# Kernel tuning notes

Measured on AMD Instinct MI355X. Metric: run time of the kernel, lower is better.

## Reference

```python
import jax, jax.numpy as jnp
import numpy as np

D_MODEL = 1024
N_HEADS = 16
CAUSAL = True
NEG_INF = -1e10


def get_freqs(seq_len, n_dim):
    # standard RoPE frequencies: theta_i = 10000^(-2i/n_dim), angles[s, i] = s * theta_i
    inv_freq = 1.0 / (10000.0 ** (jnp.arange(0, n_dim, 2, dtype=jnp.float32) / n_dim))
    t = jnp.arange(seq_len, dtype=jnp.float32)
    return jnp.outer(t, inv_freq)  # [S, n_dim//2]


def rope(x, freqs):
    # x: [B, S, H, n_dim]; interleaved pair rotation
    B, S, H, Dh = x.shape
    xr = x.reshape(B, S, H, Dh // 2, 2)
    x1, x2 = xr[..., 0], xr[..., 1]
    cos = jnp.cos(freqs)[None, :, None, :]  # [1,S,1,Dh/2]
    sin = jnp.sin(freqs)[None, :, None, :]
    o1 = x1 * cos - x2 * sin
    o2 = x1 * sin + x2 * cos
    return jnp.stack([o1, o2], axis=-1).reshape(B, S, H, Dh)


def setup_inputs() -> dict:
    key = jax.random.key(0)
    ks = jax.random.split(key, 5)
    B, S, D = 2, 2048, D_MODEL
    return {
        "x": jax.random.normal(ks[0], (B, S, D), dtype=jnp.float32),
        "qw": jax.random.normal(ks[1], (D, D), dtype=jnp.float32),
        "kw": jax.random.normal(ks[2], (D, D), dtype=jnp.float32),
        "vw": jax.random.normal(ks[3], (D, D), dtype=jnp.float32),
        "ow": jax.random.normal(ks[4], (D, D), dtype=jnp.float32),
    }


def reference(x, qw, kw, vw, ow):
    B, S, D = x.shape
    H = N_HEADS
    Dh = D // H
    Q = (x @ qw).reshape(B, S, H, Dh)
    K = (x @ kw).reshape(B, S, H, Dh)
    V = (x @ vw).reshape(B, S, H, Dh)
    freqs = get_freqs(S, Dh)
    Q = rope(Q, freqs)
    K = rope(K, freqs)
    # [B,H,S,S] scores, scaled by sqrt(d_model) as in the original (not sqrt(head_dim))
    scores = jnp.einsum("bqhd,bkhd->bhqk", Q, K) / jnp.sqrt(jnp.float32(D))
    scores = scores.astype(jnp.float32)
    if CAUSAL:
        causal = jnp.tril(jnp.ones((S, S), dtype=bool))
        scores = jnp.where(causal[None, None, :, :], scores, NEG_INF)
    weights = jax.nn.softmax(scores, axis=-1)
    attn = jnp.einsum("bhqk,bkhd->bqhd", weights, V).reshape(B, S, D)
    return attn @ ow
```

## Files before the change

### kernel.cpp

```cpp
#include <hip/hip_runtime.h>
#include <hip/hip_bf16.h>
#include <math.h>

#define SEQ    2048
#define BATCH  2
#define DM     1024
#define NH     16
#define DH     64
#define BS_ROWS 4096
#define KDIM   1024

typedef __attribute__((ext_vector_type(8))) short short8v;
typedef __attribute__((ext_vector_type(4))) float f32x4;
typedef unsigned short ushort_t;

__device__ __forceinline__ unsigned short f2bf(float f) {
  union { float f; unsigned u; } v; v.f = f;
  unsigned r = (v.u + 0x7FFF + ((v.u >> 16) & 1)) >> 16;
  return (unsigned short)r;
}
__device__ __forceinline__ float bf2f(unsigned short h) {
  union { unsigned u; float f; } v; v.u = ((unsigned)h) << 16;
  return v.f;
}

__device__ __forceinline__ void gl16(const void* g, void* l) {
  __builtin_amdgcn_global_load_lds(
      (const __attribute__((address_space(1))) unsigned int*)g,
      (__attribute__((address_space(3))) unsigned int*)l,
      16, 0, 0);
}

__global__ __launch_bounds__(256)
void split_f32(const float* __restrict__ src, ushort_t* __restrict__ h,
               ushort_t* __restrict__ l, int n8)
{
  const int i = blockIdx.x * 256 + threadIdx.x;
  if (i >= n8) return;
  const float4 v0 = ((const float4*)src)[2 * i];
  const float4 v1 = ((const float4*)src)[2 * i + 1];
  const float vals[8] = {v0.x, v0.y, v0.z, v0.w, v1.x, v1.y, v1.z, v1.w};
  short8v hv, lv;
  #pragma unroll
  for (int e = 0; e < 8; e++) {
    const unsigned short hb = f2bf(vals[e]);
    hv[e] = (short)hb;
    lv[e] = (short)f2bf(vals[e] - bf2f(hb));
  }
  ((short8v*)h)[i] = hv;
  ((short8v*)l)[i] = lv;
}

__global__ __launch_bounds__(256)
void wtrans(const float* __restrict__ w0, const float* __restrict__ w1,
            const float* __restrict__ w2, const float* __restrict__ w3,
            ushort_t* __restrict__ WT)
{
  __shared__ float tile[64][65];
  const int z = blockIdx.z;
  const float* __restrict__ W = (z == 0) ? w0 : (z == 1) ? w1 : (z == 2) ? w2 : w3;
  ushort_t* __restrict__ Oh = WT + (size_t)z * 2097152;
  ushort_t* __restrict__ Ol = Oh + 1048576;

  const int n0 = blockIdx.x * 64, k0 = blockIdx.y * 64;
  const int r  = threadIdx.x >> 2;
  const int c0 = (threadIdx.x & 3) * 16;

  #pragma unroll
  for (int i = 0; i < 4; i++) {
    const float4 v = *(const float4*)&W[(size_t)(k0 + r) * KDIM + n0 + c0 + 4 * i];
    tile[r][c0 + 4 * i + 0] = v.x; tile[r][c0 + 4 * i + 1] = v.y;
    tile[r][c0 + 4 * i + 2] = v.z; tile[r][c0 + 4 * i + 3] = v.w;
  }
  __syncthreads();

  #pragma unroll
  for (int c = 0; c < 2; c++) {
    short8v hv, lv;
    #pragma unroll
    for (int e = 0; e < 8; e++) {
      const float x = tile[c0 + c * 8 + e][r];
      const unsigned short hb = f2bf(x);
      hv[e] = (short)hb;
      lv[e] = (short)f2bf(x - bf2f(hb));
    }
    const size_t off = (size_t)(n0 + r) * KDIM + k0 + c0 + c * 8;
    *(short8v*)&Oh[off] = hv;
    if (z <= 1) *(short8v*)&Ol[off] = lv;
  }
}

#define MF(a_, b_, c_) __builtin_amdgcn_mfma_f32_16x16x32_bf16(a_, b_, c_, 0, 0, 0)

#define M16(p_, q_)                                                          \
  c00=MF(p_##0,q_##0,c00); c01=MF(p_##0,q_##1,c01); c02=MF(p_##0,q_##2,c02); c03=MF(p_##0,q_##3,c03); \
  c10=MF(p_##1,q_##0,c10); c11=MF(p_##1,q_##1,c11); c12=MF(p_##1,q_##2,c12); c13=MF(p_##1,q_##3,c13); \
  c20=MF(p_##2,q_##0,c20); c21=MF(p_##2,q_##1,c21); c22=MF(p_##2,q_##2,c22); c23=MF(p_##2,q_##3,c23); \
  c30=MF(p_##3,q_##0,c30); c31=MF(p_##3,q_##1,c31); c32=MF(p_##3,q_##2,c32); c33=MF(p_##3,q_##3,c33);

__global__ __launch_bounds__(256, 2)
void gemm_qkv(const ushort_t* __restrict__ Ahp, const ushort_t* __restrict__ Alp,
              const ushort_t* __restrict__ WT,
              ushort_t* __restrict__ Qh, ushort_t* __restrict__ Ql,
              ushort_t* __restrict__ Kh, ushort_t* __restrict__ Kl,
              ushort_t* __restrict__ Vt)
{
  const int mode = blockIdx.z;
  const bool qk = (mode <= 1);
  const ushort_t* __restrict__ Bhp = WT + (size_t)mode * 2097152;
  const ushort_t* __restrict__ Blp = Bhp + 1048576;

  __shared__ ushort_t A2[128][64];
  __shared__ ushort_t B2[128][64];

  const int t = threadIdx.x;
  const int lane = t & 63, w = t >> 6;
  const int l4 = lane & 15, lh = lane >> 4;
  const int wm = w >> 1, wn = w & 1;

  const int lin = blockIdx.x + (blockIdx.y << 3);
  const int sw  = ((lin & 7) << 5) + (lin >> 3);
  const int row0 = (sw >> 3) * 128, col0 = (sw & 7) * 128;

  const int srow = t >> 3;
  const int spc  = t & 7;
  const int slc  = spc ^ (srow & 7);
  const int koff = (slc & 3) * 8;
  const ushort_t* __restrict__ sA = (slc < 4) ? Ahp : Alp;
  const ushort_t* __restrict__ sB = (slc < 4) ? Bhp : (qk ? Blp : Bhp);

  const int pcA = lh ^ (l4 & 7);

  f32x4 c00 = {0,0,0,0}, c01 = {0,0,0,0}, c02 = {0,0,0,0}, c03 = {0,0,0,0};
  f32x4 c10 = {0,0,0,0}, c11 = {0,0,0,0}, c12 = {0,0,0,0}, c13 = {0,0,0,0};
  f32x4 c20 = {0,0,0,0}, c21 = {0,0,0,0}, c22 = {0,0,0,0}, c23 = {0,0,0,0};
  f32x4 c30 = {0,0,0,0}, c31 = {0,0,0,0}, c32 = {0,0,0,0}, c33 = {0,0,0,0};

  const int rA = wm * 64 + l4;
  const int rB = wn * 64 + l4;

  const bool stageMe = qk || (slc < 4);

  for (int k0 = 0; k0 < KDIM; k0 += 32) {
    if (stageMe) {
      #pragma unroll
      for (int i = 0; i < 4; i++) {
        gl16(sA + (size_t)(row0 + i * 32 + srow) * KDIM + k0 + koff,
             (char*)A2 + i * 4096 + w * 1024);
        gl16(sB + (size_t)(col0 + i * 32 + srow) * KDIM + k0 + koff,
             (char*)B2 + i * 4096 + w * 1024);
      }
    }
    __syncthreads();

    const short8v ah0 = *(const short8v*)&A2[rA +  0][pcA * 8];
    const short8v ah1 = *(const short8v*)&A2[rA + 16][pcA * 8];
    const short8v ah2 = *(const short8v*)&A2[rA + 32][pcA * 8];
    const short8v ah3 = *(const short8v*)&A2[rA + 48][pcA * 8];
    const short8v bh0 = *(const short8v*)&B2[rB +  0][pcA * 8];
    const short8v bh1 = *(const short8v*)&B2[rB + 16][pcA * 8];
    const short8v bh2 = *(const short8v*)&B2[rB + 32][pcA * 8];
    const short8v bh3 = *(const short8v*)&B2[rB + 48][pcA * 8];

    M16(ah, bh)
    if (qk) {
      const short8v al0 = *(const short8v*)&A2[rA +  0][(pcA ^ 4) * 8];
      const short8v al1 = *(const short8v*)&A2[rA + 16][(pcA ^ 4) * 8];
      const short8v al2 = *(const short8v*)&A2[rA + 32][(pcA ^ 4) * 8];
      const short8v al3 = *(const short8v*)&A2[rA + 48][(pcA ^ 4) * 8];
      const short8v bl0 = *(const short8v*)&B2[rB +  0][(pcA ^ 4) * 8];
      const short8v bl1 = *(const short8v*)&B2[rB + 16][(pcA ^ 4) * 8];
      const short8v bl2 = *(const short8v*)&B2[rB + 32][(pcA ^ 4) * 8];
      const short8v bl3 = *(const short8v*)&B2[rB + 48][(pcA ^ 4) * 8];
      M16(ah, bl)
      M16(al, bh)
    }
    __syncthreads();
  }

  f32x4 acc[4][4];
  acc[0][0]=c00; acc[0][1]=c01; acc[0][2]=c02; acc[0][3]=c03;
  acc[1][0]=c10; acc[1][1]=c11; acc[1][2]=c12; acc[1][3]=c13;
  acc[2][0]=c20; acc[2][1]=c21; acc[2][2]=c22; acc[2][3]=c23;
  acc[3][0]=c30; acc[3][1]=c31; acc[3][2]=c32; acc[3][3]=c33;

  if (mode <= 1) {
    const float scale = (mode == 0) ? 0.03125f : 1.0f;
    ushort_t* __restrict__ Hp = (mode == 0) ? Qh : Kh;
    ushort_t* __restrict__ Lp = (mode == 0) ? Ql : Kl;
    #pragma unroll
    for (int mf = 0; mf < 4; mf++)
      #pragma unroll
      for (int nf = 0; nf < 4; nf++) {
        const int col = col0 + wn * 64 + nf * 16 + l4;
        const int p = (col & (DH - 1)) >> 1;
        const float fr = exp2f((float)p * -0.41524101186092030f);
        const float sgn = (col & 1) ? 1.0f : -1.0f;
        #pragma unroll
        for (int j = 0; j < 4; j++) {
          const int grow = row0 + wm * 64 + mf * 16 + lh * 4 + j;
          const float s = (float)(grow & (SEQ - 1));
          float sn, cs;
          sincosf(s * fr, &sn, &cs);
          const float val = acc[mf][nf][j];
          const float par = __shfl_xor(val, 1);
          const float out = val * cs + par * (sgn * sn);
          const float xsc = out * scale;
          const unsigned short hb = f2bf(xsc);
          Hp[(size_t)grow * DM + col] = hb;
          Lp[(size_t)grow * DM + col] = f2bf(xsc - bf2f(hb));
        }
      }
  } else {
    #pragma unroll
    for (int mf = 0; mf < 4; mf++)
      #pragma unroll
      for (int nf = 0; nf < 4; nf++) {
        const int col = col0 + wn * 64 + nf * 16 + l4;
        const int hh = col >> 6, dd = col & (DH - 1);
        #pragma unroll
        for (int j = 0; j < 4; j++) {
          const int grow = row0 + wm * 64 + mf * 16 + lh * 4 + j;
          const int b = grow >> 11, ss = grow & (SEQ - 1);
          Vt[((size_t)((b * NH + hh) * DH + dd)) * SEQ + ss] = f2bf(acc[mf][nf][j]);
        }
      }
  }
}

__global__ __launch_bounds__(256, 2)
void gemm_out(const ushort_t* __restrict__ Ahp, const ushort_t* __restrict__ WT,
              float* __restrict__ Cf)
{
  const ushort_t* __restrict__ Bhp = WT + (size_t)3 * 2097152;

  __shared__ ushort_t A3[128][32];
  __shared__ ushort_t B3[64][32];

  const int t = threadIdx.x;
  const int lane = t & 63, w = t >> 6;
  const int l4 = lane & 15, lh = lane >> 4;
  const int wm = w >> 1, wn = w & 1;

  const int lin = blockIdx.x + (blockIdx.y << 4);
  const int sw  = ((lin & 7) << 6) + (lin >> 3);
  const int row0 = (sw >> 4) * 128, col0 = (sw & 15) * 64;

  const int srow = t >> 2;
  const int spc  = t & 3;
  const int slc  = spc ^ (srow & 3);
  const int koff = slc * 8;

  const int pc4 = lh ^ (l4 & 3);

  f32x4 c00={0,0,0,0}, c01={0,0,0,0};
  f32x4 c10={0,0,0,0}, c11={0,0,0,0};
  f32x4 c20={0,0,0,0}, c21={0,0,0,0};
  f32x4 c30={0,0,0,0}, c31={0,0,0,0};

  const int rA = wm * 64 + l4;
  const int rB = wn * 32 + l4;

  for (int k0 = 0; k0 < KDIM; k0 += 32) {
    #pragma unroll
    for (int i = 0; i < 2; i++)
      gl16(Ahp + (size_t)(row0 + i * 64 + srow) * KDIM + k0 + koff,
           (char*)A3 + i * 4096 + w * 1024);
    gl16(Bhp + (size_t)(col0 + srow) * KDIM + k0 + koff,
         (char*)B3 + w * 1024);
    __syncthreads();

    const short8v ah0 = *(const short8v*)&A3[rA +  0][pc4 * 8];
    const short8v ah1 = *(const short8v*)&A3[rA + 16][pc4 * 8];
    const short8v ah2 = *(const short8v*)&A3[rA + 32][pc4 * 8];
    const short8v ah3 = *(const short8v*)&A3[rA + 48][pc4 * 8];
    const short8v bh0 = *(const short8v*)&B3[rB +  0][pc4 * 8];
    const short8v bh1 = *(const short8v*)&B3[rB + 16][pc4 * 8];

    c00 = MF(ah0, bh0, c00); c01 = MF(ah0, bh1, c01);
    c10 = MF(ah1, bh0, c10); c11 = MF(ah1, bh1, c11);
    c20 = MF(ah2, bh0, c20); c21 = MF(ah2, bh1, c21);
    c30 = MF(ah3, bh0, c30); c31 = MF(ah3, bh1, c31);
    __syncthreads();
  }

  f32x4 acc[4][2];
  acc[0][0]=c00; acc[0][1]=c01; acc[1][0]=c10; acc[1][1]=c11;
  acc[2][0]=c20; acc[2][1]=c21; acc[3][0]=c30; acc[3][1]=c31;

  #pragma unroll
  for (int mf = 0; mf < 4; mf++)
    #pragma unroll
    for (int nf = 0; nf < 2; nf++) {
      const int col = col0 + wn * 32 + nf * 16 + l4;
      #pragma unroll
      for (int j = 0; j < 4; j++) {
        const int grow = row0 + wm * 64 + mf * 16 + lh * 4 + j;
        Cf[(size_t)grow * DM + col] = acc[mf][nf][j];
      }
    }
}

__global__ __launch_bounds__(256, 4)
void attn_mfma(const ushort_t* __restrict__ Qh, const ushort_t* __restrict__ Ql,
               const ushort_t* __restrict__ Kh, const ushort_t* __restrict__ Kl,
               const ushort_t* __restrict__ Vt, ushort_t* __restrict__ AAh)
{
  __shared__ __align__(16) ushort_t Khl[2][2][64][32];
  __shared__ __align__(16) ushort_t Vtl[64][72];
  __shared__ __align__(16) ushort_t Pl[4][16][72];

  const int t = threadIdx.x;
  const int lane = t & 63, wv = t >> 6;
  const int l4 = lane & 15, lh = lane >> 4;

  const int lin = blockIdx.x + (blockIdx.y << 5);
  const int sw  = ((lin & 7) << 7) + (lin >> 3);
  const int qblk = sw & 31, bh = sw >> 5;

  const int bI = bh >> 4, h = bh & 15;
  const int q0w = qblk * 64 + wv * 16;
  const int qrow = q0w + l4;

  const int kr = t >> 2, kc = t & 3;
  const int ckw = (kc ^ ((kr >> 1) & 3)) * 8;
  const int csr = (lh ^ ((l4 >> 1) & 3)) * 8;

  short8v aqh0, aqh1, aql0, aql1;
  {
    const size_t qoff = (size_t)((bI * SEQ) + qrow) * DM + h * DH;
    aqh0 = *(const short8v*)&Qh[qoff + lh * 8];
    aqh1 = *(const short8v*)&Qh[qoff + 32 + lh * 8];
    aql0 = *(const short8v*)&Ql[qoff + lh * 8];
    aql1 = *(const short8v*)&Ql[qoff + 32 + lh * 8];
  }

  f32x4 o0 = {0,0,0,0}, o1 = {0,0,0,0}, o2 = {0,0,0,0}, o3 = {0,0,0,0};
  float mrun = -1e30f, lsum = 0.f;

  const ushort_t* __restrict__ Vg = Vt + (size_t)bh * DH * SEQ;
  const size_t kgbase = (size_t)(bI * SEQ + kr) * DM + h * DH + kc * 8;
  const int nt = qblk + 1;

  short8v rkh0, rkh1, rkl0, rkl1, rv0, rv1;

#define LOADR(kt_) {                                                         \
    const size_t ko = kgbase + (size_t)(kt_) * 64 * DM;                      \
    rkh0 = *(const short8v*)&Kh[ko];                                         \
    rkh1 = *(const short8v*)&Kh[ko + 32];                                    \
    rkl0 = *(const short8v*)&Kl[ko];                                         \
    rkl1 = *(const short8v*)&Kl[ko + 32];                                    \
    const size_t vo = (size_t)kr * SEQ + (kt_) * 64 + kc * 8;                \
    rv0 = *(const short8v*)&Vg[vo];                                          \
    rv1 = *(const short8v*)&Vg[vo + 32]; }

#define WRITES() {                                                           \
    *(short8v*)&Khl[0][0][kr][ckw] = rkh0;                                   \
    *(short8v*)&Khl[0][1][kr][ckw] = rkh1;                                   \
    *(short8v*)&Khl[1][0][kr][ckw] = rkl0;                                   \
    *(short8v*)&Khl[1][1][kr][ckw] = rkl1;                                   \
    *(short8v*)&Vtl[kr][kc * 8]      = rv0;                                  \
    *(short8v*)&Vtl[kr][kc * 8 + 32] = rv1; }

#define QKSTEP(sN, n) {                                                      \
    const short8v kh0 = *(const short8v*)&Khl[0][0][(n)*16 + l4][csr];       \
    const short8v kh1 = *(const short8v*)&Khl[0][1][(n)*16 + l4][csr];       \
    const short8v kl0 = *(const short8v*)&Khl[1][0][(n)*16 + l4][csr];       \
    const short8v kl1 = *(const short8v*)&Khl[1][1][(n)*16 + l4][csr];       \
    sN = MF(kh0, aqh0, sN);                                                  \
    sN = MF(kh0, aql0, sN);                                                  \
    sN = MF(kl0, aqh0, sN);                                                  \
    sN = MF(kh1, aqh1, sN);                                                  \
    sN = MF(kh1, aql1, sN);                                                  \
    sN = MF(kl1, aqh1, sN); }

#define MASKN(sN, n) {                                                       \
    const int kb0 = kb + (n)*16 + lh*4;                                      \
    if (kb0 + 0 > qrow) sN[0] = -1e30f;                                      \
    if (kb0 + 1 > qrow) sN[1] = -1e30f;                                      \
    if (kb0 + 2 > qrow) sN[2] = -1e30f;                                      \
    if (kb0 + 3 > qrow) sN[3] = -1e30f; }

#define EXPN(sN) {                                                           \
    sN[0] = __expf(sN[0] - nm); sN[1] = __expf(sN[1] - nm);                  \
    sN[2] = __expf(sN[2] - nm); sN[3] = __expf(sN[3] - nm); }

#define PWRITE(sN, n) {                                                      \
    unsigned pa, pb;                                                         \
    asm("v_cvt_pk_bf16_f32 %0, %1, %2" : "=v"(pa) : "v"(sN[0]), "v"(sN[1]));\
    asm("v_cvt_pk_bf16_f32 %0, %1, %2" : "=v"(pb) : "v"(sN[2]), "v"(sN[3]));\
    *(unsigned*)&Pl[wv][l4][(n)*16 + lh*4]     = pa;                         \
    *(unsigned*)&Pl[wv][l4][(n)*16 + lh*4 + 2] = pb; }

#define PVSTEP(kb2) {                                                        \
    const short8v ap  = *(const short8v*)&Pl[wv][l4][(kb2)*32 + lh*8];       \
    const short8v bv0 = *(const short8v*)&Vtl[ 0 + l4][(kb2)*32 + lh*8];     \
    const short8v bv1 = *(const short8v*)&Vtl[16 + l4][(kb2)*32 + lh*8];     \
    const short8v bv2 = *(const short8v*)&Vtl[32 + l4][(kb2)*32 + lh*8];     \
    const short8v bv3 = *(const short8v*)&Vtl[48 + l4][(kb2)*32 + lh*8];     \
    o0 = MF(bv0, ap, o0);                                                    \
    o1 = MF(bv1, ap, o1);                                                    \
    o2 = MF(bv2, ap, o2);                                                    \
    o3 = MF(bv3, ap, o3); }

  LOADR(0); WRITES();
  __syncthreads();

  for (int kt = 0; kt < nt; kt++) {
    const bool pf = (kt + 1 < nt);
    if (pf) LOADR(kt + 1);

    f32x4 s0 = {0,0,0,0}, s1 = {0,0,0,0}, s2 = {0,0,0,0}, s3 = {0,0,0,0};
    QKSTEP(s0, 0) QKSTEP(s1, 1) QKSTEP(s2, 2) QKSTEP(s3, 3)

    const int kb = kt * 64;
    MASKN(s0, 0) MASKN(s1, 1) MASKN(s2, 2) MASKN(s3, 3)

    float vmax = fmaxf(fmaxf(fmaxf(s0[0], s0[1]), fmaxf(s0[2], s0[3])),
                       fmaxf(fmaxf(s1[0], s1[1]), fmaxf(s1[2], s1[3])));
    vmax = fmaxf(vmax, fmaxf(fmaxf(s2[0], s2[1]), fmaxf(s2[2], s2[3])));
    vmax = fmaxf(vmax, fmaxf(fmaxf(s3[0], s3[1]), fmaxf(s3[2], s3[3])));
    vmax = fmaxf(vmax, __shfl_xor(vmax, 16));
    vmax = fmaxf(vmax, __shfl_xor(vmax, 32));

    float nm = fmaxf(mrun, vmax);
    if (__all(nm - mrun <= 8.0f)) {
      nm = mrun;
    } else {
      const float corr = __expf(mrun - nm);
      lsum *= corr;
      o0 *= corr; o1 *= corr; o2 *= corr; o3 *= corr;
      mrun = nm;
    }

    EXPN(s0) EXPN(s1) EXPN(s2) EXPN(s3)

    float rs = (s0[0] + s0[1]) + (s0[2] + s0[3]) + (s1[0] + s1[1]) + (s1[2] + s1[3])
             + (s2[0] + s2[1]) + (s2[2] + s2[3]) + (s3[0] + s3[1]) + (s3[2] + s3[3]);
    rs += __shfl_xor(rs, 16);
    rs += __shfl_xor(rs, 32);
    lsum += rs;

    PWRITE(s0, 0) PWRITE(s1, 1) PWRITE(s2, 2) PWRITE(s3, 3)

    PVSTEP(0) PVSTEP(1)

    if (pf) {
      __syncthreads();
      WRITES();
      __syncthreads();
    }
  }

  const float inv = 1.0f / lsum;
  const size_t rowoff = ((size_t)(bI * SEQ + qrow)) * DM + h * DH;
  #pragma unroll
  for (int df = 0; df < 4; df++) {
    const f32x4 ov = (df == 0) ? o0 : (df == 1) ? o1 : (df == 2) ? o2 : o3;
    #pragma unroll
    for (int jp = 0; jp < 2; jp++) {
      const float x0 = ov[2 * jp] * inv;
      const float x1 = ov[2 * jp + 1] * inv;
      const unsigned short h0 = f2bf(x0), h1 = f2bf(x1);
      const size_t col = rowoff + df * 16 + lh * 4 + 2 * jp;
      *(unsigned*)&AAh[col] = (unsigned)h0 | ((unsigned)h1 << 16);
    }
  }
#undef LOADR
#undef WRITES
#undef QKSTEP
#undef MASKN
#undef EXPN
#undef PWRITE
#undef PVSTEP
}

extern "C" void kernel_launch(void* const* d_in, const int* in_sizes, int n_in,
                              void* d_out, int out_size, void* d_ws, size_t ws_size,
                              hipStream_t stream) {
  const float* x  = (const float*)d_in[0];
  const float* qw = (const float*)d_in[1];
  const float* kw = (const float*)d_in[2];
  const float* vw = (const float*)d_in[3];
  const float* ow = (const float*)d_in[4];

  char* ws = (char*)d_ws;
  ushort_t* Xh  = (ushort_t*)ws;
  ushort_t* Xl  = Xh + 4194304;
  ushort_t* AAh = Xh;
  ushort_t* Kh  = (ushort_t*)(ws + (16u << 20));
  ushort_t* Kl  = Kh + 4194304;
  ushort_t* Vt  = (ushort_t*)(ws + (32u << 20));
  ushort_t* WT  = (ushort_t*)(ws + (40u << 20));
  ushort_t* Qh  = (ushort_t*)d_out;
  ushort_t* Ql  = Qh + 4194304;
  float*    out = (float*)d_out;

  split_f32<<<dim3(2048), dim3(256), 0, stream>>>(x, Xh, Xl, 524288);
  wtrans<<<dim3(16, 16, 4), dim3(256), 0, stream>>>(qw, kw, vw, ow, WT);
  gemm_qkv<<<dim3(8, 32, 3), dim3(256), 0, stream>>>(
      Xh, Xl, WT, Qh, Ql, Kh, Kl, Vt);
  attn_mfma<<<dim3(SEQ / 64, BATCH * NH), dim3(256), 0, stream>>>(
      Qh, Ql, Kh, Kl, Vt, AAh);
  gemm_out<<<dim3(16, 32), dim3(256), 0, stream>>>(AAh, WT, out);
}
```

Baseline: 199.0 us.

## Shrink QKV GEMM tile to 64x128 and add MFMA priority hints in attention

The QKV projection GEMM moves from 128x128 tiles with a 2x2 warp layout to 64x128 tiles with four warps split along N. Each warp now holds 8 accumulators instead of 16, launch bounds rise to 4 blocks per CU, and the grid doubles. The aim is higher occupancy and better load balance, at the cost of less reuse of the staged B tile and more global loads overall. Separately, the attention kernel wraps its QK and PV MFMA sections in s_setprio to favour matrix issue over other waves.

```diff
diff --git a/kernel.cpp b/kernel.cpp
--- a/kernel.cpp
+++ b/kernel.cpp
@@ -92,13 +92,7 @@
 
 #define MF(a_, b_, c_) __builtin_amdgcn_mfma_f32_16x16x32_bf16(a_, b_, c_, 0, 0, 0)
 
-#define M16(p_, q_)                                                          \
-  c00=MF(p_##0,q_##0,c00); c01=MF(p_##0,q_##1,c01); c02=MF(p_##0,q_##2,c02); c03=MF(p_##0,q_##3,c03); \
-  c10=MF(p_##1,q_##0,c10); c11=MF(p_##1,q_##1,c11); c12=MF(p_##1,q_##2,c12); c13=MF(p_##1,q_##3,c13); \
-  c20=MF(p_##2,q_##0,c20); c21=MF(p_##2,q_##1,c21); c22=MF(p_##2,q_##2,c22); c23=MF(p_##2,q_##3,c23); \
-  c30=MF(p_##3,q_##0,c30); c31=MF(p_##3,q_##1,c31); c32=MF(p_##3,q_##2,c32); c33=MF(p_##3,q_##3,c33);
-
-__global__ __launch_bounds__(256, 2)
+__global__ __launch_bounds__(256, 4)
 void gemm_qkv(const ushort_t* __restrict__ Ahp, const ushort_t* __restrict__ Alp,
               const ushort_t* __restrict__ WT,
               ushort_t* __restrict__ Qh, ushort_t* __restrict__ Ql,
@@ -110,95 +104,101 @@
   const ushort_t* __restrict__ Bhp = WT + (size_t)mode * 2097152;
   const ushort_t* __restrict__ Blp = Bhp + 1048576;
 
-  __shared__ ushort_t A2[128][64];
+  __shared__ ushort_t A2[64][64];
   __shared__ ushort_t B2[128][64];
 
   const int t = threadIdx.x;
   const int lane = t & 63, w = t >> 6;
   const int l4 = lane & 15, lh = lane >> 4;
-  const int wm = w >> 1, wn = w & 1;
+  const int wn = w;
 
   const int lin = blockIdx.x + (blockIdx.y << 3);
-  const int sw  = ((lin & 7) << 5) + (lin >> 3);
-  const int row0 = (sw >> 3) * 128, col0 = (sw & 7) * 128;
+  const int sw  = ((lin & 7) << 6) + (lin >> 3);
+  const int row0 = (sw >> 3) * 64, col0 = (sw & 7) * 128;
 
   const int srow = t >> 3;
   const int spc  = t & 7;
   const int slc  = spc ^ (srow & 7);
   const int koff = (slc & 3) * 8;
   const ushort_t* __restrict__ sA = (slc < 4) ? Ahp : Alp;
-  const ushort_t* __restrict__ sB = (slc < 4) ? Bhp : (qk ? Blp : Bhp);
+  const ushort_t* __restrict__ sB = (slc < 4) ? Bhp : Blp;
+  const bool stageMe = qk || (slc < 4);
 
   const int pcA = lh ^ (l4 & 7);
 
-  f32x4 c00 = {0,0,0,0}, c01 = {0,0,0,0}, c02 = {0,0,0,0}, c03 = {0,0,0,0};
-  f32x4 c10 = {0,0,0,0}, c11 = {0,0,0,0}, c12 = {0,0,0,0}, c13 = {0,0,0,0};
-  f32x4 c20 = {0,0,0,0}, c21 = {0,0,0,0}, c22 = {0,0,0,0}, c23 = {0,0,0,0};
-  f32x4 c30 = {0,0,0,0}, c31 = {0,0,0,0}, c32 = {0,0,0,0}, c33 = {0,0,0,0};
-
-  const int rA = wm * 64 + l4;
-  const int rB = wn * 64 + l4;
-
-  const bool stageMe = qk || (slc < 4);
+  f32x4 c00 = {0,0,0,0}, c01 = {0,0,0,0};
+  f32x4 c10 = {0,0,0,0}, c11 = {0,0,0,0};
+  f32x4 c20 = {0,0,0,0}, c21 = {0,0,0,0};
+  f32x4 c30 = {0,0,0,0}, c31 = {0,0,0,0};
+
+  const int rB0 = wn * 32 + l4;
+  const int rB1 = wn * 32 + 16 + l4;
 
   for (int k0 = 0; k0 < KDIM; k0 += 32) {
     if (stageMe) {
       #pragma unroll
-      for (int i = 0; i < 4; i++) {
+      for (int i = 0; i < 2; i++)
         gl16(sA + (size_t)(row0 + i * 32 + srow) * KDIM + k0 + koff,
              (char*)A2 + i * 4096 + w * 1024);
+      #pragma unroll
+      for (int i = 0; i < 4; i++)
         gl16(sB + (size_t)(col0 + i * 32 + srow) * KDIM + k0 + koff,
              (char*)B2 + i * 4096 + w * 1024);
-      }
     }
     __syncthreads();
 
-    const short8v ah0 = *(const short8v*)&A2[rA +  0][pcA * 8];
-    const short8v ah1 = *(const short8v*)&A2[rA + 16][pcA * 8];
-    const short8v ah2 = *(const short8v*)&A2[rA + 32][pcA * 8];
-    const short8v ah3 = *(const short8v*)&A2[rA + 48][pcA * 8];
-    const short8v bh0 = *(const short8v*)&B2[rB +  0][pcA * 8];
-    const short8v bh1 = *(const short8v*)&B2[rB + 16][pcA * 8];
-    const short8v bh2 = *(const short8v*)&B2[rB + 32][pcA * 8];
-    const short8v bh3 = *(const short8v*)&B2[rB + 48][pcA * 8];
-
-    M16(ah, bh)
+    const short8v ah0 = *(const short8v*)&A2[ 0 + l4][pcA * 8];
+    const short8v ah1 = *(const short8v*)&A2[16 + l4][pcA * 8];
+    const short8v ah2 = *(const short8v*)&A2[32 + l4][pcA * 8];
+    const short8v ah3 = *(const short8v*)&A2[48 + l4][pcA * 8];
+    const short8v bh0 = *(const short8v*)&B2[rB0][pcA * 8];
+    const short8v bh1 = *(const short8v*)&B2[rB1][pcA * 8];
+
+    c00 = MF(ah0, bh0, c00); c01 = MF(ah0, bh1, c01);
+    c10 = MF(ah1, bh0, c10); c11 = MF(ah1, bh1, c11);
+    c20 = MF(ah2, bh0, c20); c21 = MF(ah2, bh1, c21);
+    c30 = MF(ah3, bh0, c30); c31 = MF(ah3, bh1, c31);
+
     if (qk) {
-      const short8v al0 = *(const short8v*)&A2[rA +  0][(pcA ^ 4) * 8];
-      const short8v al1 = *(const short8v*)&A2[rA + 16][(pcA ^ 4) * 8];
-      const short8v al2 = *(const short8v*)&A2[rA + 32][(pcA ^ 4) * 8];
-      const short8v al3 = *(const short8v*)&A2[rA + 48][(pcA ^ 4) * 8];
-      const short8v bl0 = *(const short8v*)&B2[rB +  0][(pcA ^ 4) * 8];
-      const short8v bl1 = *(const short8v*)&B2[rB + 16][(pcA ^ 4) * 8];
-      const short8v bl2 = *(const short8v*)&B2[rB + 32][(pcA ^ 4) * 8];
-      const short8v bl3 = *(const short8v*)&B2[rB + 48][(pcA ^ 4) * 8];
-      M16(ah, bl)
-      M16(al, bh)
+      const short8v al0 = *(const short8v*)&A2[ 0 + l4][(pcA ^ 4) * 8];
+      const short8v al1 = *(const short8v*)&A2[16 + l4][(pcA ^ 4) * 8];
+      const short8v al2 = *(const short8v*)&A2[32 + l4][(pcA ^ 4) * 8];
+      const short8v al3 = *(const short8v*)&A2[48 + l4][(pcA ^ 4) * 8];
+      const short8v bl0 = *(const short8v*)&B2[rB0][(pcA ^ 4) * 8];
+      const short8v bl1 = *(const short8v*)&B2[rB1][(pcA ^ 4) * 8];
+
+      c00 = MF(ah0, bl0, c00); c01 = MF(ah0, bl1, c01);
+      c10 = MF(ah1, bl0, c10); c11 = MF(ah1, bl1, c11);
+      c20 = MF(ah2, bl0, c20); c21 = MF(ah2, bl1, c21);
+      c30 = MF(ah3, bl0, c30); c31 = MF(ah3, bl1, c31);
+
+      c00 = MF(al0, bh0, c00); c01 = MF(al0, bh1, c01);
+      c10 = MF(al1, bh0, c10); c11 = MF(al1, bh1, c11);
+      c20 = MF(al2, bh0, c20); c21 = MF(al2, bh1, c21);
+      c30 = MF(al3, bh0, c30); c31 = MF(al3, bh1, c31);
     }
     __syncthreads();
   }
 
-  f32x4 acc[4][4];
-  acc[0][0]=c00; acc[0][1]=c01; acc[0][2]=c02; acc[0][3]=c03;
-  acc[1][0]=c10; acc[1][1]=c11; acc[1][2]=c12; acc[1][3]=c13;
-  acc[2][0]=c20; acc[2][1]=c21; acc[2][2]=c22; acc[2][3]=c23;
-  acc[3][0]=c30; acc[3][1]=c31; acc[3][2]=c32; acc[3][3]=c33;
+  f32x4 acc[4][2];
+  acc[0][0]=c00; acc[0][1]=c01; acc[1][0]=c10; acc[1][1]=c11;
+  acc[2][0]=c20; acc[2][1]=c21; acc[3][0]=c30; acc[3][1]=c31;
 
   if (mode <= 1) {
     const float scale = (mode == 0) ? 0.03125f : 1.0f;
     ushort_t* __restrict__ Hp = (mode == 0) ? Qh : Kh;
     ushort_t* __restrict__ Lp = (mode == 0) ? Ql : Kl;
     #pragma unroll
-    for (int mf = 0; mf < 4; mf++)
+    for (int nf = 0; nf < 2; nf++) {
+      const int col = col0 + wn * 32 + nf * 16 + l4;
+      const int p = (col & (DH - 1)) >> 1;
+      const float fr = exp2f((float)p * -0.41524101186092030f);
+      const float sgn = (col & 1) ? 1.0f : -1.0f;
       #pragma unroll
-      for (int nf = 0; nf < 4; nf++) {
-        const int col = col0 + wn * 64 + nf * 16 + l4;
-        const int p = (col & (DH - 1)) >> 1;
-        const float fr = exp2f((float)p * -0.41524101186092030f);
-        const float sgn = (col & 1) ? 1.0f : -1.0f;
+      for (int mf = 0; mf < 4; mf++) {
         #pragma unroll
         for (int j = 0; j < 4; j++) {
-          const int grow = row0 + wm * 64 + mf * 16 + lh * 4 + j;
+          const int grow = row0 + mf * 16 + lh * 4 + j;
           const float s = (float)(grow & (SEQ - 1));
           float sn, cs;
           sincosf(s * fr, &sn, &cs);
@@ -211,20 +211,22 @@
           Lp[(size_t)grow * DM + col] = f2bf(xsc - bf2f(hb));
         }
       }
+    }
   } else {
     #pragma unroll
-    for (int mf = 0; mf < 4; mf++)
+    for (int nf = 0; nf < 2; nf++) {
+      const int col = col0 + wn * 32 + nf * 16 + l4;
+      const int hh = col >> 6, dd = col & (DH - 1);
       #pragma unroll
-      for (int nf = 0; nf < 4; nf++) {
-        const int col = col0 + wn * 64 + nf * 16 + l4;
-        const int hh = col >> 6, dd = col & (DH - 1);
+      for (int mf = 0; mf < 4; mf++) {
         #pragma unroll
         for (int j = 0; j < 4; j++) {
-          const int grow = row0 + wm * 64 + mf * 16 + lh * 4 + j;
+          const int grow = row0 + mf * 16 + lh * 4 + j;
           const int b = grow >> 11, ss = grow & (SEQ - 1);
           Vt[((size_t)((b * NH + hh) * DH + dd)) * SEQ + ss] = f2bf(acc[mf][nf][j]);
         }
       }
+    }
   }
 }
 
@@ -411,7 +413,9 @@
     if (pf) LOADR(kt + 1);
 
     f32x4 s0 = {0,0,0,0}, s1 = {0,0,0,0}, s2 = {0,0,0,0}, s3 = {0,0,0,0};
+    __builtin_amdgcn_s_setprio(1);
     QKSTEP(s0, 0) QKSTEP(s1, 1) QKSTEP(s2, 2) QKSTEP(s3, 3)
+    __builtin_amdgcn_s_setprio(0);
 
     const int kb = kt * 64;
     MASKN(s0, 0) MASKN(s1, 1) MASKN(s2, 2) MASKN(s3, 3)
@@ -443,7 +447,9 @@
 
     PWRITE(s0, 0) PWRITE(s1, 1) PWRITE(s2, 2) PWRITE(s3, 3)
 
+    __builtin_amdgcn_s_setprio(1);
     PVSTEP(0) PVSTEP(1)
+    __builtin_amdgcn_s_setprio(0);
 
     if (pf) {
       __syncthreads();
@@ -498,7 +504,7 @@
 
   split_f32<<<dim3(2048), dim3(256), 0, stream>>>(x, Xh, Xl, 524288);
   wtrans<<<dim3(16, 16, 4), dim3(256), 0, stream>>>(qw, kw, vw, ow, WT);
-  gemm_qkv<<<dim3(8, 32, 3), dim3(256), 0, stream>>>(
+  gemm_qkv<<<dim3(8, 64, 3), dim3(256), 0, stream>>>(
       Xh, Xl, WT, Qh, Ql, Kh, Kl, Vt);
   attn_mfma<<<dim3(SEQ / 64, BATCH * NH), dim3(256), 0, stream>>>(
       Qh, Ql, Kh, Kl, Vt, AAh);
```

After: 199.7 us. About the same (+0.4%).

## Merge prologue kernels, fold log2e into Q scale, add MFMA priority hints

Applied to the files above, without the earlier changes.

Combines the input split and weight transpose kernels into a single launch so one kernel launch and its gap go away. Folds log2(e) into the Q scale so softmax can use exp2f directly and skip the multiply inside __expf, with the rescale threshold adjusted to match. Wraps the QK and PV MFMA sections in s_setprio to favour matrix-issuing waves. Folding the constant into the bf16-split Q values may shift rounding slightly.

```diff
diff --git a/kernel.cpp b/kernel.cpp
--- a/kernel.cpp
+++ b/kernel.cpp
@@ -32,37 +32,41 @@
 }
 
 __global__ __launch_bounds__(256)
-void split_f32(const float* __restrict__ src, ushort_t* __restrict__ h,
-               ushort_t* __restrict__ l, int n8)
-{
-  const int i = blockIdx.x * 256 + threadIdx.x;
-  if (i >= n8) return;
-  const float4 v0 = ((const float4*)src)[2 * i];
-  const float4 v1 = ((const float4*)src)[2 * i + 1];
-  const float vals[8] = {v0.x, v0.y, v0.z, v0.w, v1.x, v1.y, v1.z, v1.w};
-  short8v hv, lv;
-  #pragma unroll
-  for (int e = 0; e < 8; e++) {
-    const unsigned short hb = f2bf(vals[e]);
-    hv[e] = (short)hb;
-    lv[e] = (short)f2bf(vals[e] - bf2f(hb));
-  }
-  ((short8v*)h)[i] = hv;
-  ((short8v*)l)[i] = lv;
-}
-
-__global__ __launch_bounds__(256)
-void wtrans(const float* __restrict__ w0, const float* __restrict__ w1,
-            const float* __restrict__ w2, const float* __restrict__ w3,
-            ushort_t* __restrict__ WT)
+void prologue(const float* __restrict__ x,
+              const float* __restrict__ w0, const float* __restrict__ w1,
+              const float* __restrict__ w2, const float* __restrict__ w3,
+              ushort_t* __restrict__ Xh, ushort_t* __restrict__ Xl,
+              ushort_t* __restrict__ WT)
 {
   __shared__ float tile[64][65];
-  const int z = blockIdx.z;
+  const int bid = blockIdx.x;
+
+  if (bid < 2048) {
+    const int i = bid * 256 + threadIdx.x;
+    const float4 v0 = ((const float4*)x)[2 * i];
+    const float4 v1 = ((const float4*)x)[2 * i + 1];
+    const float vals[8] = {v0.x, v0.y, v0.z, v0.w, v1.x, v1.y, v1.z, v1.w};
+    short8v hv, lv;
+    #pragma unroll
+    for (int e = 0; e < 8; e++) {
+      const unsigned short hb = f2bf(vals[e]);
+      hv[e] = (short)hb;
+      lv[e] = (short)f2bf(vals[e] - bf2f(hb));
+    }
+    ((short8v*)Xh)[i] = hv;
+    ((short8v*)Xl)[i] = lv;
+    return;
+  }
+
+  const int bid2 = bid - 2048;
+  const int z = bid2 >> 8;
+  const int rem = bid2 & 255;
+  const int n0 = (rem & 15) * 64, k0 = (rem >> 4) * 64;
+
   const float* __restrict__ W = (z == 0) ? w0 : (z == 1) ? w1 : (z == 2) ? w2 : w3;
   ushort_t* __restrict__ Oh = WT + (size_t)z * 2097152;
   ushort_t* __restrict__ Ol = Oh + 1048576;
 
-  const int n0 = blockIdx.x * 64, k0 = blockIdx.y * 64;
   const int r  = threadIdx.x >> 2;
   const int c0 = (threadIdx.x & 3) * 16;
 
@@ -79,10 +83,10 @@
     short8v hv, lv;
     #pragma unroll
     for (int e = 0; e < 8; e++) {
-      const float x = tile[c0 + c * 8 + e][r];
-      const unsigned short hb = f2bf(x);
+      const float xx = tile[c0 + c * 8 + e][r];
+      const unsigned short hb = f2bf(xx);
       hv[e] = (short)hb;
-      lv[e] = (short)f2bf(x - bf2f(hb));
+      lv[e] = (short)f2bf(xx - bf2f(hb));
     }
     const size_t off = (size_t)(n0 + r) * KDIM + k0 + c0 + c * 8;
     *(short8v*)&Oh[off] = hv;
@@ -185,7 +189,7 @@
   acc[3][0]=c30; acc[3][1]=c31; acc[3][2]=c32; acc[3][3]=c33;
 
   if (mode <= 1) {
-    const float scale = (mode == 0) ? 0.03125f : 1.0f;
+    const float scale = (mode == 0) ? 0.04508422002778011f : 1.0f;
     ushort_t* __restrict__ Hp = (mode == 0) ? Qh : Kh;
     ushort_t* __restrict__ Lp = (mode == 0) ? Ql : Kl;
     #pragma unroll
@@ -382,8 +386,8 @@
     if (kb0 + 3 > qrow) sN[3] = -1e30f; }
 
 #define EXPN(sN) {                                                           \
-    sN[0] = __expf(sN[0] - nm); sN[1] = __expf(sN[1] - nm);                  \
-    sN[2] = __expf(sN[2] - nm); sN[3] = __expf(sN[3] - nm); }
+    sN[0] = exp2f(sN[0] - nm); sN[1] = exp2f(sN[1] - nm);                    \
+    sN[2] = exp2f(sN[2] - nm); sN[3] = exp2f(sN[3] - nm); }
 
 #define PWRITE(sN, n) {                                                      \
     unsigned pa, pb;                                                         \
@@ -411,7 +415,9 @@
     if (pf) LOADR(kt + 1);
 
     f32x4 s0 = {0,0,0,0}, s1 = {0,0,0,0}, s2 = {0,0,0,0}, s3 = {0,0,0,0};
+    __builtin_amdgcn_s_setprio(1);
     QKSTEP(s0, 0) QKSTEP(s1, 1) QKSTEP(s2, 2) QKSTEP(s3, 3)
+    __builtin_amdgcn_s_setprio(0);
 
     const int kb = kt * 64;
     MASKN(s0, 0) MASKN(s1, 1) MASKN(s2, 2) MASKN(s3, 3)
@@ -424,10 +430,10 @@
     vmax = fmaxf(vmax, __shfl_xor(vmax, 32));
 
     float nm = fmaxf(mrun, vmax);
-    if (__all(nm - mrun <= 8.0f)) {
+    if (__all(nm - mrun <= 11.5415603f)) {
       nm = mrun;
     } else {
-      const float corr = __expf(mrun - nm);
+      const float corr = exp2f(mrun - nm);
       lsum *= corr;
       o0 *= corr; o1 *= corr; o2 *= corr; o3 *= corr;
       mrun = nm;
@@ -443,7 +449,9 @@
 
     PWRITE(s0, 0) PWRITE(s1, 1) PWRITE(s2, 2) PWRITE(s3, 3)
 
+    __builtin_amdgcn_s_setprio(1);
     PVSTEP(0) PVSTEP(1)
+    __builtin_amdgcn_s_setprio(0);
 
     if (pf) {
       __syncthreads();
@@ -496,8 +504,7 @@
   ushort_t* Ql  = Qh + 4194304;
   float*    out = (float*)d_out;
 
-  split_f32<<<dim3(2048), dim3(256), 0, stream>>>(x, Xh, Xl, 524288);
-  wtrans<<<dim3(16, 16, 4), dim3(256), 0, stream>>>(qw, kw, vw, ow, WT);
+  prologue<<<dim3(3072), dim3(256), 0, stream>>>(x, qw, kw, vw, ow, Xh, Xl, WT);
   gemm_qkv<<<dim3(8, 32, 3), dim3(256), 0, stream>>>(
       Xh, Xl, WT, Qh, Ql, Kh, Kl, Vt);
   attn_mfma<<<dim3(SEQ / 64, BATCH * NH), dim3(256), 0, stream>>>(
```

Measured after the change: 202.2 us. Within noise of the previous version (+1.6%).
